# Performance work log

Measured on AMD Instinct MI355X. Metric: run time of the kernel, lower is better.

Reference implementation:

```python
import jax, jax.numpy as jnp
import numpy as np
import math

D_MODEL = 512
N_HEADS = 8
WINDOW = 5
B, S = 4, 2048


def setup_inputs() -> dict:
    key = jax.random.key(0)
    ks = jax.random.split(key, 16)
    d = D_MODEL

    def lin(k, fan_in, fan_out):
        bound = 1.0 / math.sqrt(fan_in)
        kw, kb = jax.random.split(k)
        W = jax.random.uniform(kw, (fan_in, fan_out), jnp.float32, -bound, bound)
        b = jax.random.uniform(kb, (fan_out,), jnp.float32, -bound, bound)
        return W, b

    x = jax.random.normal(ks[0], (B, S, d), jnp.float32)
    W1, b1 = lin(ks[1], d, 2 * d)      # mapping layer 1
    W2, b2 = lin(ks[2], 2 * d, d)      # mapping layer 2
    Wq, bq = lin(ks[3], d, d)
    Wk, bk = lin(ks[4], d, d)
    Wv, bv = lin(ks[5], d, d)
    Wo, bo = lin(ks[6], d, d)
    return dict(x=x, W1=W1, b1=b1, W2=W2, b2=b2, Wq=Wq, bq=bq,
                Wk=Wk, bk=bk, Wv=Wv, bv=bv, Wo=Wo, bo=bo)


def reference(x, W1, b1, W2, b2, Wq, bq, Wk, bk, Wv, bv, Wo, bo):
    Bsz, S_, d = x.shape
    h = N_HEADS
    hd = d // h

    # mapping MLP: Linear -> ReLU -> Linear
    xm = jax.nn.relu(x @ W1 + b1) @ W2 + b2

    def split_heads(t):  # [B,S,d] -> [B,h,S,hd]
        return t.reshape(Bsz, S_, h, hd).transpose(0, 2, 1, 3)

    Q = split_heads(xm @ Wq + bq)
    K = split_heads(xm @ Wk + bk)
    V = split_heads(xm @ Wv + bv)

    scores = jnp.einsum('bhqd,bhkd->bhqk', Q, K) / math.sqrt(hd)

    # inverse sliding-window mask: positions with |i-j| <= window are EXCLUDED
    idx = jnp.arange(S_)
    adjacent = jnp.abs(idx[:, None] - idx[None, :]) <= WINDOW  # [S,S] bool
    scores = jnp.where(adjacent[None, None], -1e9, scores)

    attn = jax.nn.softmax(scores, axis=-1)
    out = jnp.einsum('bhqk,bhkd->bhqd', attn, V)
    out = out.transpose(0, 2, 1, 3).reshape(Bsz, S_, d)
    return out @ Wo + bo
```

## Files before the change

kernel.cpp:

```cpp
#include <hip/hip_runtime.h>
#include <stdint.h>

typedef __attribute__((ext_vector_type(8))) short bf16x8;
typedef __attribute__((ext_vector_type(4))) float f32x4;

__device__ __forceinline__ float bf2f(uint16_t u) {
    union { uint32_t u; float f; } c; c.u = ((uint32_t)u) << 16; return c.f;
}
__device__ __forceinline__ uint16_t f2bf(float f) {
    union { float f; uint32_t u; } c; c.f = f;
    uint32_t r = c.u + 0x7fffu + ((c.u >> 16) & 1u);
    return (uint16_t)(r >> 16);
}
__device__ __forceinline__ uint32_t pk2bf(float a, float b) {
#if __has_builtin(__builtin_amdgcn_cvt_pk_bf16_f32)
    auto v = __builtin_amdgcn_cvt_pk_bf16_f32(a, b);
    uint32_t u; __builtin_memcpy(&u, &v, 4); return u;
#else
    return (uint32_t)f2bf(a) | ((uint32_t)f2bf(b) << 16);
#endif
}

__device__ __forceinline__ void gld_lds16(const uint16_t* g, uint16_t* l) {
    __builtin_amdgcn_global_load_lds(
        (const __attribute__((address_space(1))) void*)g,
        (__attribute__((address_space(3))) void*)l, 16, 0, 0);
}

__global__ void prep_all(const float* __restrict__ x,
                         const float* __restrict__ W1, const float* __restrict__ W2,
                         const float* __restrict__ Wq, const float* __restrict__ Wk,
                         const float* __restrict__ Wv, const float* __restrict__ Wo,
                         const float* __restrict__ b1, const float* __restrict__ b2,
                         const float* __restrict__ bq, const float* __restrict__ bk,
                         const float* __restrict__ bv, const float* __restrict__ bo,
                         uint16_t* __restrict__ W1T, uint16_t* __restrict__ W2T,
                         uint16_t* __restrict__ WqkvT, uint16_t* __restrict__ WoT,
                         uint16_t* __restrict__ xb, uint16_t* __restrict__ bbase)
{
    const int id = blockIdx.x;
    const int tx = threadIdx.x, ty = threadIdx.y;
    const int tid = ty * 32 + tx;
    if (id < 2048) {
        __shared__ uint16_t t[32][33];
        const float* src; uint16_t* dst; int R, C, tile;
        if      (id < 512)  { src = W1; dst = W1T;              R = 512;  C = 1024; tile = id; }
        else if (id < 1024) { src = W2; dst = W2T;              R = 1024; C = 512;  tile = id - 512; }
        else if (id < 1280) { src = Wq; dst = WqkvT;            R = 512;  C = 512;  tile = id - 1024; }
        else if (id < 1536) { src = Wk; dst = WqkvT + 512*512;  R = 512;  C = 512;  tile = id - 1280; }
        else if (id < 1792) { src = Wv; dst = WqkvT + 1024*512; R = 512;  C = 512;  tile = id - 1536; }
        else                { src = Wo; dst = WoT;              R = 512;  C = 512;  tile = id - 1792; }
        const int ntx = C / 32;
        const int bx = (tile % ntx) * 32, by = (tile / ntx) * 32;
#pragma unroll
        for (int i = ty; i < 32; i += 8) t[i][tx] = f2bf(src[(size_t)(by + i) * C + bx + tx]);
        __syncthreads();
#pragma unroll
        for (int i = ty; i < 32; i += 8) dst[(size_t)(bx + i) * R + by + tx] = t[tx][i];
    } else if (id < 6144) {
        int i = (id - 2048) * 256 + tid;
        float4 v = ((const float4*)x)[i];
        ushort4 o;
        o.x = f2bf(v.x); o.y = f2bf(v.y); o.z = f2bf(v.z); o.w = f2bf(v.w);
        ((ushort4*)xb)[i] = o;
    } else {
        int i = (id - 6144) * 256 + tid;
        if      (i < 1024) bbase[i] = f2bf(b1[i]);
        else if (i < 1536) bbase[i] = f2bf(b2[i - 1024]);
        else if (i < 2048) bbase[i] = f2bf(bq[i - 1536]);
        else if (i < 2560) bbase[i] = f2bf(bk[i - 2048]);
        else if (i < 3072) bbase[i] = f2bf(bv[i - 2560]);
        else if (i < 3584) bbase[i] = f2bf(bo[i - 3072]);
    }
}

template<int RELU, int F32OUT>
__global__ __launch_bounds__(256)
void gemm_k(const uint16_t* __restrict__ A, const uint16_t* __restrict__ Bt,
            const uint16_t* __restrict__ bias, void* __restrict__ Cv,
            int M, int N, int K)
{
    __shared__ __align__(16) uint16_t lsA[128 * 32];
    __shared__ __align__(16) uint16_t lsB[128 * 32];

    const int tid = threadIdx.x, lane = tid & 63, wid = tid >> 6;
    const int quad = lane >> 4, lm = lane & 15;
    const int wm = wid >> 1, wn = wid & 1;
    const int m0 = blockIdx.y * 128, n0 = blockIdx.x * 128;

    f32x4 acc[4][4];
#pragma unroll
    for (int i = 0; i < 4; ++i)
#pragma unroll
        for (int j = 0; j < 4; ++j) acc[i][j] = (f32x4){0.f, 0.f, 0.f, 0.f};

    const int row0 = tid >> 2, row1 = (256 + tid) >> 2, cg = tid & 3;

    for (int k0 = 0; k0 < K; k0 += 32) {
        __syncthreads();
        gld_lds16(A  + (size_t)(m0 + row0) * K + k0 + cg * 8, lsA + (size_t)tid * 8);
        gld_lds16(A  + (size_t)(m0 + row1) * K + k0 + cg * 8, lsA + (size_t)(256 + tid) * 8);
        gld_lds16(Bt + (size_t)(n0 + row0) * K + k0 + cg * 8, lsB + (size_t)tid * 8);
        gld_lds16(Bt + (size_t)(n0 + row1) * K + k0 + cg * 8, lsB + (size_t)(256 + tid) * 8);
        __syncthreads();

        bf16x8 af[4], bfr[4];
#pragma unroll
        for (int t = 0; t < 4; ++t) {
            af[t]  = *(const bf16x8*)(lsA + (wm * 64 + t * 16 + lm) * 32 + quad * 8);
            bfr[t] = *(const bf16x8*)(lsB + (wn * 64 + t * 16 + lm) * 32 + quad * 8);
        }
#pragma unroll
        for (int i = 0; i < 4; ++i)
#pragma unroll
            for (int j = 0; j < 4; ++j)
                acc[i][j] = __builtin_amdgcn_mfma_f32_16x16x32_bf16(af[i], bfr[j], acc[i][j], 0, 0, 0);
    }

#pragma unroll
    for (int i = 0; i < 4; ++i) {
        const int r0 = m0 + wm * 64 + i * 16 + quad * 4;
#pragma unroll
        for (int j = 0; j < 4; ++j) {
            const int col = n0 + wn * 64 + j * 16 + lm;
            const float bvj = bf2f(bias[col]);
#pragma unroll
            for (int r = 0; r < 4; ++r) {
                float v = acc[i][j][r] + bvj;
                if (RELU) v = fmaxf(v, 0.f);
                if (F32OUT) ((float*)Cv)[(size_t)(r0 + r) * N + col] = v;
                else        ((uint16_t*)Cv)[(size_t)(r0 + r) * N + col] = f2bf(v);
            }
        }
    }
}

template<int RELU, int F32OUT>
__global__ __launch_bounds__(256)
void gemm_k64(const uint16_t* __restrict__ A, const uint16_t* __restrict__ Bt,
              const uint16_t* __restrict__ bias, void* __restrict__ Cv,
              int M, int N, int K)
{
    __shared__ __align__(16) uint16_t lsA[64 * 32];
    __shared__ __align__(16) uint16_t lsB[128 * 32];

    const int tid = threadIdx.x, lane = tid & 63, wid = tid >> 6;
    const int quad = lane >> 4, lm = lane & 15;
    const int wm = wid >> 1, wn = wid & 1;
    const int m0 = blockIdx.y * 64, n0 = blockIdx.x * 128;

    f32x4 acc[2][4];
#pragma unroll
    for (int i = 0; i < 2; ++i)
#pragma unroll
        for (int j = 0; j < 4; ++j) acc[i][j] = (f32x4){0.f, 0.f, 0.f, 0.f};

    const int rowA = tid >> 2;
    const int rowB0 = tid >> 2, rowB1 = (256 + tid) >> 2, cg = tid & 3;

    for (int k0 = 0; k0 < K; k0 += 32) {
        __syncthreads();
        gld_lds16(A  + (size_t)(m0 + rowA) * K + k0 + cg * 8, lsA + (size_t)tid * 8);
        gld_lds16(Bt + (size_t)(n0 + rowB0) * K + k0 + cg * 8, lsB + (size_t)tid * 8);
        gld_lds16(Bt + (size_t)(n0 + rowB1) * K + k0 + cg * 8, lsB + (size_t)(256 + tid) * 8);
        __syncthreads();

        bf16x8 af[2], bfr[4];
#pragma unroll
        for (int t = 0; t < 2; ++t)
            af[t] = *(const bf16x8*)(lsA + (wm * 32 + t * 16 + lm) * 32 + quad * 8);
#pragma unroll
        for (int t = 0; t < 4; ++t)
            bfr[t] = *(const bf16x8*)(lsB + (wn * 64 + t * 16 + lm) * 32 + quad * 8);
#pragma unroll
        for (int i = 0; i < 2; ++i)
#pragma unroll
            for (int j = 0; j < 4; ++j)
                acc[i][j] = __builtin_amdgcn_mfma_f32_16x16x32_bf16(af[i], bfr[j], acc[i][j], 0, 0, 0);
    }

#pragma unroll
    for (int i = 0; i < 2; ++i) {
        const int r0 = m0 + wm * 32 + i * 16 + quad * 4;
#pragma unroll
        for (int j = 0; j < 4; ++j) {
            const int col = n0 + wn * 64 + j * 16 + lm;
            const float bvj = bf2f(bias[col]);
#pragma unroll
            for (int r = 0; r < 4; ++r) {
                float v = acc[i][j][r] + bvj;
                if (RELU) v = fmaxf(v, 0.f);
                if (F32OUT) ((float*)Cv)[(size_t)(r0 + r) * N + col] = v;
                else        ((uint16_t*)Cv)[(size_t)(r0 + r) * N + col] = f2bf(v);
            }
        }
    }
}

__global__ __launch_bounds__(256)
void gemm_qkv_s(const uint16_t* __restrict__ A, const uint16_t* __restrict__ Bt,
                const uint16_t* __restrict__ bq, const uint16_t* __restrict__ bk,
                const uint16_t* __restrict__ bv_,
                uint16_t* __restrict__ qk, uint16_t* __restrict__ Vt)
{
    __shared__ __align__(16) uint16_t lsA[128 * 32];
    __shared__ __align__(16) uint16_t lsB[128 * 32];

    const int tid = threadIdx.x, lane = tid & 63, wid = tid >> 6;
    const int quad = lane >> 4, lm = lane & 15;
    const int wm = wid >> 1, wn = wid & 1;
    const int m0 = blockIdx.y * 128, n0 = blockIdx.x * 128;
    const int part = n0 >> 9;
    const uint16_t* B = (part == 0) ? bq : (part == 1) ? bk : bv_;
    const int K = 512;

    f32x4 acc[4][4];
#pragma unroll
    for (int i = 0; i < 4; ++i)
#pragma unroll
        for (int j = 0; j < 4; ++j) acc[i][j] = (f32x4){0.f, 0.f, 0.f, 0.f};

    const int row0 = tid >> 2, row1 = (256 + tid) >> 2, cg = tid & 3;

    for (int k0 = 0; k0 < K; k0 += 32) {
        __syncthreads();
        gld_lds16(A  + (size_t)(m0 + row0) * K + k0 + cg * 8, lsA + (size_t)tid * 8);
        gld_lds16(A  + (size_t)(m0 + row1) * K + k0 + cg * 8, lsA + (size_t)(256 + tid) * 8);
        gld_lds16(Bt + (size_t)(n0 + row0) * K + k0 + cg * 8, lsB + (size_t)tid * 8);
        gld_lds16(Bt + (size_t)(n0 + row1) * K + k0 + cg * 8, lsB + (size_t)(256 + tid) * 8);
        __syncthreads();

        bf16x8 af[4], bfr[4];
#pragma unroll
        for (int t = 0; t < 4; ++t) {
            af[t]  = *(const bf16x8*)(lsA + (wm * 64 + t * 16 + lm) * 32 + quad * 8);
            bfr[t] = *(const bf16x8*)(lsB + (wn * 64 + t * 16 + lm) * 32 + quad * 8);
        }
#pragma unroll
        for (int i = 0; i < 4; ++i)
#pragma unroll
            for (int j = 0; j < 4; ++j)
                acc[i][j] = __builtin_amdgcn_mfma_f32_16x16x32_bf16(af[i], bfr[j], acc[i][j], 0, 0, 0);
    }

#pragma unroll
    for (int i = 0; i < 4; ++i) {
        const int mb = m0 + wm * 64 + i * 16 + quad * 4;
#pragma unroll
        for (int j = 0; j < 4; ++j) {
            const int nl = (n0 & 511) + wn * 64 + j * 16 + lm;
            const float bvj = bf2f(B[nl]);
            if (part < 2) {
#pragma unroll
                for (int r = 0; r < 4; ++r)
                    qk[(size_t)(mb + r) * 1024 + part * 512 + nl] = f2bf(acc[i][j][r] + bvj);
            } else {
                const int h = nl >> 6, d = nl & 63;
                const int b = mb >> 11, s0 = mb & 2047;
                const size_t base = ((size_t)(((b << 3) | h)) * 64 + d) * 2048 + s0;
#pragma unroll
                for (int r = 0; r < 4; ++r)
                    Vt[base + r] = f2bf(acc[i][j][r] + bvj);
            }
        }
    }
}

__global__ __launch_bounds__(256, 2)
void attn_k(const uint16_t* __restrict__ qk, const uint16_t* __restrict__ Vt,
            uint16_t* __restrict__ Out)
{
    __shared__ __align__(16) uint16_t lsK[128 * 64];
    __shared__ __align__(16) uint16_t lsV[64 * 128];
    __shared__ __align__(16) uint16_t lsP[128 * 136];

    const int tid = threadIdx.x, lane = tid & 63, wid = tid >> 6;
    const int quad = lane >> 4, lm = lane & 15;
    const int bh = blockIdx.y, b = bh >> 3, h = bh & 7;
    const int q0 = blockIdx.x * 128;
    const float cscale = 0.125f * 1.44269504088896f;

    bf16x8 qf[2][2];
#pragma unroll
    for (int i = 0; i < 2; ++i)
#pragma unroll
        for (int ks = 0; ks < 2; ++ks) {
            bf16x8 q = *(const bf16x8*)(qk +
                (size_t)(b * 2048 + q0 + wid * 32 + i * 16 + lm) * 1024 + h * 64 + ks * 32 + quad * 8);
#pragma unroll
            for (int e = 0; e < 8; ++e)
                q[e] = (short)f2bf(bf2f((uint16_t)q[e]) * cscale);
            qf[i][ks] = q;
        }

    f32x4 oacc[2][4];
#pragma unroll
    for (int i = 0; i < 2; ++i)
#pragma unroll
        for (int n = 0; n < 4; ++n) oacc[i][n] = (f32x4){0.f, 0.f, 0.f, 0.f};
    float lrow[2][4];
#pragma unroll
    for (int i = 0; i < 2; ++i)
#pragma unroll
        for (int r = 0; r < 4; ++r) lrow[i][r] = 0.f;

    for (int j0 = 0; j0 < 2048; j0 += 128) {
        __syncthreads();
#pragma unroll
        for (int c4 = 0; c4 < 4; ++c4) {
            const int chunk = c4 * 256 + tid;
            const int r = chunk >> 3, lc = (chunk & 7) ^ (r & 7);
            gld_lds16(qk + (size_t)(b * 2048 + j0 + r) * 1024 + 512 + h * 64 + lc * 8,
                      lsK + (size_t)chunk * 8);
        }
#pragma unroll
        for (int c4 = 0; c4 < 4; ++c4) {
            const int chunk = c4 * 256 + tid;
            const int d = chunk >> 4, lc = (chunk & 15) ^ (d & 15);
            gld_lds16(Vt + (size_t)(bh * 64 + d) * 2048 + j0 + lc * 8,
                      lsV + (size_t)chunk * 8);
        }
        __syncthreads();

        f32x4 sacc[2][8];
#pragma unroll
        for (int i = 0; i < 2; ++i)
#pragma unroll
            for (int j = 0; j < 8; ++j) sacc[i][j] = (f32x4){0.f, 0.f, 0.f, 0.f};
#pragma unroll
        for (int ks = 0; ks < 2; ++ks)
#pragma unroll
            for (int j = 0; j < 8; ++j) {
                const int pc = (ks * 4 + quad) ^ (lm & 7);
                bf16x8 kf = *(const bf16x8*)(lsK + (j * 16 + lm) * 64 + pc * 8);
#pragma unroll
                for (int i = 0; i < 2; ++i)
                    sacc[i][j] = __builtin_amdgcn_mfma_f32_16x16x32_bf16(qf[i][ks], kf, sacc[i][j], 0, 0, 0);
            }

        if ((j0 + 127 >= q0 - 5) && (j0 <= q0 + 127 + 5)) {
#pragma unroll
            for (int i = 0; i < 2; ++i)
#pragma unroll
                for (int j = 0; j < 8; ++j)
#pragma unroll
                    for (int r = 0; r < 4; ++r) {
                        int qr = q0 + wid * 32 + i * 16 + quad * 4 + r;
                        int kc = j0 + j * 16 + lm;
                        int dd = qr - kc; if (dd < 0) dd = -dd;
                        if (dd <= 5) sacc[i][j][r] = -1e30f;
                    }
        }

#pragma unroll
        for (int i = 0; i < 2; ++i)
#pragma unroll
            for (int r = 0; r < 4; ++r) {
                const int prow = wid * 32 + i * 16 + quad * 4 + r;
                float p[8], rs = 0.f;
#pragma unroll
                for (int j = 0; j < 8; ++j) { p[j] = exp2f(sacc[i][j][r]); rs += p[j]; }
                lrow[i][r] += rs;
#pragma unroll
                for (int jp = 0; jp < 4; ++jp) {
                    uint32_t u = pk2bf(p[2 * jp], p[2 * jp + 1]);
                    lsP[prow * 136 + (2 * jp) * 16 + lm]     = (uint16_t)u;
                    lsP[prow * 136 + (2 * jp + 1) * 16 + lm] = (uint16_t)(u >> 16);
                }
            }

#pragma unroll
        for (int ks = 0; ks < 4; ++ks) {
            bf16x8 pa[2];
#pragma unroll
            for (int i = 0; i < 2; ++i)
                pa[i] = *(const bf16x8*)(lsP + (wid * 32 + i * 16 + lm) * 136 + ks * 32 + quad * 8);
#pragma unroll
            for (int n = 0; n < 4; ++n) {
                const int pc = (ks * 4 + quad) ^ lm;
                bf16x8 vf = *(const bf16x8*)(lsV + (n * 16 + lm) * 128 + pc * 8);
#pragma unroll
                for (int i = 0; i < 2; ++i)
                    oacc[i][n] = __builtin_amdgcn_mfma_f32_16x16x32_bf16(pa[i], vf, oacc[i][n], 0, 0, 0);
            }
        }
    }

#pragma unroll
    for (int i = 0; i < 2; ++i)
#pragma unroll
        for (int r = 0; r < 4; ++r) {
            float l = lrow[i][r];
            l += __shfl_xor(l, 1, 16);
            l += __shfl_xor(l, 2, 16);
            l += __shfl_xor(l, 4, 16);
            l += __shfl_xor(l, 8, 16);
            const float inv = 1.f / (l + 1e-30f);
            const int s = q0 + wid * 32 + i * 16 + quad * 4 + r;
#pragma unroll
            for (int n = 0; n < 4; ++n)
                Out[(size_t)(b * 2048 + s) * 512 + h * 64 + n * 16 + lm] = f2bf(oacc[i][n][r] * inv);
        }
}

extern "C" void kernel_launch(void* const* d_in, const int* in_sizes, int n_in,
                              void* d_out, int out_size, void* d_ws, size_t ws_size,
                              hipStream_t stream)
{
    const float* x  = (const float*)d_in[0];
    const float* W1 = (const float*)d_in[1];
    const float* b1 = (const float*)d_in[2];
    const float* W2 = (const float*)d_in[3];
    const float* b2 = (const float*)d_in[4];
    const float* Wq = (const float*)d_in[5];
    const float* bq = (const float*)d_in[6];
    const float* Wk = (const float*)d_in[7];
    const float* bk = (const float*)d_in[8];
    const float* Wv = (const float*)d_in[9];
    const float* bv = (const float*)d_in[10];
    const float* Wo = (const float*)d_in[11];
    const float* bo = (const float*)d_in[12];
    (void)in_sizes; (void)n_in; (void)out_size; (void)ws_size;

    char* ws = (char*)d_ws;
    const size_t MiB = 1024 * 1024;
    uint16_t* xb    = (uint16_t*)(ws + 0);
    uint16_t* W1T   = (uint16_t*)(ws + 8 * MiB);
    uint16_t* W2T   = (uint16_t*)(ws + 9 * MiB);
    uint16_t* WqkvT = (uint16_t*)(ws + 10 * MiB);
    uint16_t* WoT   = (uint16_t*)(ws + 11 * MiB + 512 * 1024);
    uint16_t* bbase = (uint16_t*)(ws + 12 * MiB);
    uint16_t* b1b = bbase, *b2b = bbase + 1024, *bqb = bbase + 1536;
    uint16_t* bkb = bbase + 2048, *bvb = bbase + 2560, *bob = bbase + 3072;
    uint16_t* xm1   = (uint16_t*)(ws + 13 * MiB);
    uint16_t* xm    = (uint16_t*)(ws + 29 * MiB);
    uint16_t* qk    = xm1;
    uint16_t* att   = xm;
    uint16_t* Vt    = xb;

    prep_all<<<6158, dim3(32, 8), 0, stream>>>(x, W1, W2, Wq, Wk, Wv, Wo,
                                               b1, b2, bq, bk, bv, bo,
                                               W1T, W2T, WqkvT, WoT, xb, bbase);

    gemm_k<1,0>  <<<dim3(8, 64),  256, 0, stream>>>(xb,  W1T, b1b, xm1, 8192, 1024, 512);
    gemm_k64<0,0><<<dim3(4, 128), 256, 0, stream>>>(xm1, W2T, b2b, xm,  8192, 512, 1024);
    gemm_qkv_s   <<<dim3(12, 64), 256, 0, stream>>>(xm, WqkvT, bqb, bkb, bvb, qk, Vt);
    attn_k       <<<dim3(16, 32), 256, 0, stream>>>(qk, Vt, att);
    gemm_k64<0,1><<<dim3(4, 128), 256, 0, stream>>>(att, WoT, bob, d_out, 8192, 512, 512);
}
```

Before: 251.3 us.

## Double GEMM K-step to 64 with XOR-swizzled LDS, use native exp2

All three GEMM kernels now stage 64-wide K slices per iteration instead of 32, halving the number of barrier pairs per tile. The LDS layout is XOR-swizzled by row to avoid bank conflicts on the wider rows. The attention softmax switches to the raw hardware exp2 builtin, which skips the library's range handling. The cost is double the LDS footprint per block, which may reduce occupancy.

```diff
diff --git a/kernel.cpp b/kernel.cpp
--- a/kernel.cpp
+++ b/kernel.cpp
@@ -18,6 +18,13 @@
     uint32_t u; __builtin_memcpy(&u, &v, 4); return u;
 #else
     return (uint32_t)f2bf(a) | ((uint32_t)f2bf(b) << 16);
+#endif
+}
+__device__ __forceinline__ float fexp2(float x) {
+#if __has_builtin(__builtin_amdgcn_exp2f)
+    return __builtin_amdgcn_exp2f(x);
+#else
+    return exp2f(x);
 #endif
 }
 
@@ -80,10 +87,11 @@
             const uint16_t* __restrict__ bias, void* __restrict__ Cv,
             int M, int N, int K)
 {
-    __shared__ __align__(16) uint16_t lsA[128 * 32];
-    __shared__ __align__(16) uint16_t lsB[128 * 32];
-
-    const int tid = threadIdx.x, lane = tid & 63, wid = tid >> 6;
+    __shared__ __align__(16) uint16_t lsA[128 * 64];
+    __shared__ __align__(16) uint16_t lsB[128 * 64];
+
+    const int tid = threadIdx.x, lane = tid & 63;
+    const int wid = tid >> 6;
     const int quad = lane >> 4, lm = lane & 15;
     const int wm = wid >> 1, wn = wid & 1;
     const int m0 = blockIdx.y * 128, n0 = blockIdx.x * 128;
@@ -94,27 +102,32 @@
 #pragma unroll
         for (int j = 0; j < 4; ++j) acc[i][j] = (f32x4){0.f, 0.f, 0.f, 0.f};
 
-    const int row0 = tid >> 2, row1 = (256 + tid) >> 2, cg = tid & 3;
-
-    for (int k0 = 0; k0 < K; k0 += 32) {
-        __syncthreads();
-        gld_lds16(A  + (size_t)(m0 + row0) * K + k0 + cg * 8, lsA + (size_t)tid * 8);
-        gld_lds16(A  + (size_t)(m0 + row1) * K + k0 + cg * 8, lsA + (size_t)(256 + tid) * 8);
-        gld_lds16(Bt + (size_t)(n0 + row0) * K + k0 + cg * 8, lsB + (size_t)tid * 8);
-        gld_lds16(Bt + (size_t)(n0 + row1) * K + k0 + cg * 8, lsB + (size_t)(256 + tid) * 8);
-        __syncthreads();
-
-        bf16x8 af[4], bfr[4];
-#pragma unroll
-        for (int t = 0; t < 4; ++t) {
-            af[t]  = *(const bf16x8*)(lsA + (wm * 64 + t * 16 + lm) * 32 + quad * 8);
-            bfr[t] = *(const bf16x8*)(lsB + (wn * 64 + t * 16 + lm) * 32 + quad * 8);
-        }
-#pragma unroll
-        for (int i = 0; i < 4; ++i)
-#pragma unroll
-            for (int j = 0; j < 4; ++j)
-                acc[i][j] = __builtin_amdgcn_mfma_f32_16x16x32_bf16(af[i], bfr[j], acc[i][j], 0, 0, 0);
+    for (int k0 = 0; k0 < K; k0 += 64) {
+        __syncthreads();
+#pragma unroll
+        for (int c4 = 0; c4 < 4; ++c4) {
+            const int chunk = c4 * 256 + tid;
+            const int r = chunk >> 3, lc = (chunk & 7) ^ (r & 7);
+            gld_lds16(A  + (size_t)(m0 + r) * K + k0 + lc * 8, lsA + (size_t)chunk * 8);
+            gld_lds16(Bt + (size_t)(n0 + r) * K + k0 + lc * 8, lsB + (size_t)chunk * 8);
+        }
+        __syncthreads();
+
+#pragma unroll
+        for (int kh = 0; kh < 2; ++kh) {
+            bf16x8 af[4], bfr[4];
+#pragma unroll
+            for (int t = 0; t < 4; ++t) {
+                const int pcA = ((kh * 4 + quad) ^ (lm & 7));
+                af[t]  = *(const bf16x8*)(lsA + (wm * 64 + t * 16 + lm) * 64 + pcA * 8);
+                bfr[t] = *(const bf16x8*)(lsB + (wn * 64 + t * 16 + lm) * 64 + pcA * 8);
+            }
+#pragma unroll
+            for (int i = 0; i < 4; ++i)
+#pragma unroll
+                for (int j = 0; j < 4; ++j)
+                    acc[i][j] = __builtin_amdgcn_mfma_f32_16x16x32_bf16(af[i], bfr[j], acc[i][j], 0, 0, 0);
+        }
     }
 
 #pragma unroll
@@ -141,10 +154,11 @@
               const uint16_t* __restrict__ bias, void* __restrict__ Cv,
               int M, int N, int K)
 {
-    __shared__ __align__(16) uint16_t lsA[64 * 32];
-    __shared__ __align__(16) uint16_t lsB[128 * 32];
-
-    const int tid = threadIdx.x, lane = tid & 63, wid = tid >> 6;
+    __shared__ __align__(16) uint16_t lsA[64 * 64];
+    __shared__ __align__(16) uint16_t lsB[128 * 64];
+
+    const int tid = threadIdx.x, lane = tid & 63;
+    const int wid = tid >> 6;
     const int quad = lane >> 4, lm = lane & 15;
     const int wm = wid >> 1, wn = wid & 1;
     const int m0 = blockIdx.y * 64, n0 = blockIdx.x * 128;
@@ -155,28 +169,38 @@
 #pragma unroll
         for (int j = 0; j < 4; ++j) acc[i][j] = (f32x4){0.f, 0.f, 0.f, 0.f};
 
-    const int rowA = tid >> 2;
-    const int rowB0 = tid >> 2, rowB1 = (256 + tid) >> 2, cg = tid & 3;
-
-    for (int k0 = 0; k0 < K; k0 += 32) {
-        __syncthreads();
-        gld_lds16(A  + (size_t)(m0 + rowA) * K + k0 + cg * 8, lsA + (size_t)tid * 8);
-        gld_lds16(Bt + (size_t)(n0 + rowB0) * K + k0 + cg * 8, lsB + (size_t)tid * 8);
-        gld_lds16(Bt + (size_t)(n0 + rowB1) * K + k0 + cg * 8, lsB + (size_t)(256 + tid) * 8);
-        __syncthreads();
-
-        bf16x8 af[2], bfr[4];
-#pragma unroll
-        for (int t = 0; t < 2; ++t)
-            af[t] = *(const bf16x8*)(lsA + (wm * 32 + t * 16 + lm) * 32 + quad * 8);
-#pragma unroll
-        for (int t = 0; t < 4; ++t)
-            bfr[t] = *(const bf16x8*)(lsB + (wn * 64 + t * 16 + lm) * 32 + quad * 8);
-#pragma unroll
-        for (int i = 0; i < 2; ++i)
-#pragma unroll
-            for (int j = 0; j < 4; ++j)
-                acc[i][j] = __builtin_amdgcn_mfma_f32_16x16x32_bf16(af[i], bfr[j], acc[i][j], 0, 0, 0);
+    for (int k0 = 0; k0 < K; k0 += 64) {
+        __syncthreads();
+#pragma unroll
+        for (int c4 = 0; c4 < 2; ++c4) {
+            const int chunk = c4 * 256 + tid;
+            const int r = chunk >> 3, lc = (chunk & 7) ^ (r & 7);
+            gld_lds16(A + (size_t)(m0 + r) * K + k0 + lc * 8, lsA + (size_t)chunk * 8);
+        }
+#pragma unroll
+        for (int c4 = 0; c4 < 4; ++c4) {
+            const int chunk = c4 * 256 + tid;
+            const int r = chunk >> 3, lc = (chunk & 7) ^ (r & 7);
+            gld_lds16(Bt + (size_t)(n0 + r) * K + k0 + lc * 8, lsB + (size_t)chunk * 8);
+        }
+        __syncthreads();
+
+#pragma unroll
+        for (int kh = 0; kh < 2; ++kh) {
+            const int pc = ((kh * 4 + quad) ^ (lm & 7));
+            bf16x8 af[2], bfr[4];
+#pragma unroll
+            for (int t = 0; t < 2; ++t)
+                af[t] = *(const bf16x8*)(lsA + (wm * 32 + t * 16 + lm) * 64 + pc * 8);
+#pragma unroll
+            for (int t = 0; t < 4; ++t)
+                bfr[t] = *(const bf16x8*)(lsB + (wn * 64 + t * 16 + lm) * 64 + pc * 8);
+#pragma unroll
+            for (int i = 0; i < 2; ++i)
+#pragma unroll
+                for (int j = 0; j < 4; ++j)
+                    acc[i][j] = __builtin_amdgcn_mfma_f32_16x16x32_bf16(af[i], bfr[j], acc[i][j], 0, 0, 0);
+        }
     }
 
 #pragma unroll
@@ -203,10 +227,11 @@
                 const uint16_t* __restrict__ bv_,
                 uint16_t* __restrict__ qk, uint16_t* __restrict__ Vt)
 {
-    __shared__ __align__(16) uint16_t lsA[128 * 32];
-    __shared__ __align__(16) uint16_t lsB[128 * 32];
-
-    const int tid = threadIdx.x, lane = tid & 63, wid = tid >> 6;
+    __shared__ __align__(16) uint16_t lsA[128 * 64];
+    __shared__ __align__(16) uint16_t lsB[128 * 64];
+
+    const int tid = threadIdx.x, lane = tid & 63;
+    const int wid = tid >> 6;
     const int quad = lane >> 4, lm = lane & 15;
     const int wm = wid >> 1, wn = wid & 1;
     const int m0 = blockIdx.y * 128, n0 = blockIdx.x * 128;
@@ -220,27 +245,32 @@
 #pragma unroll
         for (int j = 0; j < 4; ++j) acc[i][j] = (f32x4){0.f, 0.f, 0.f, 0.f};
 
-    const int row0 = tid >> 2, row1 = (256 + tid) >> 2, cg = tid & 3;
-
-    for (int k0 = 0; k0 < K; k0 += 32) {
-        __syncthreads();
-        gld_lds16(A  + (size_t)(m0 + row0) * K + k0 + cg * 8, lsA + (size_t)tid * 8);
-        gld_lds16(A  + (size_t)(m0 + row1) * K + k0 + cg * 8, lsA + (size_t)(256 + tid) * 8);
-        gld_lds16(Bt + (size_t)(n0 + row0) * K + k0 + cg * 8, lsB + (size_t)tid * 8);
-        gld_lds16(Bt + (size_t)(n0 + row1) * K + k0 + cg * 8, lsB + (size_t)(256 + tid) * 8);
-        __syncthreads();
-
-        bf16x8 af[4], bfr[4];
-#pragma unroll
-        for (int t = 0; t < 4; ++t) {
-            af[t]  = *(const bf16x8*)(lsA + (wm * 64 + t * 16 + lm) * 32 + quad * 8);
-            bfr[t] = *(const bf16x8*)(lsB + (wn * 64 + t * 16 + lm) * 32 + quad * 8);
-        }
-#pragma unroll
-        for (int i = 0; i < 4; ++i)
-#pragma unroll
-            for (int j = 0; j < 4; ++j)
-                acc[i][j] = __builtin_amdgcn_mfma_f32_16x16x32_bf16(af[i], bfr[j], acc[i][j], 0, 0, 0);
+    for (int k0 = 0; k0 < K; k0 += 64) {
+        __syncthreads();
+#pragma unroll
+        for (int c4 = 0; c4 < 4; ++c4) {
+            const int chunk = c4 * 256 + tid;
+            const int r = chunk >> 3, lc = (chunk & 7) ^ (r & 7);
+            gld_lds16(A  + (size_t)(m0 + r) * K + k0 + lc * 8, lsA + (size_t)chunk * 8);
+            gld_lds16(Bt + (size_t)(n0 + r) * K + k0 + lc * 8, lsB + (size_t)chunk * 8);
+        }
+        __syncthreads();
+
+#pragma unroll
+        for (int kh = 0; kh < 2; ++kh) {
+            const int pc = ((kh * 4 + quad) ^ (lm & 7));
+            bf16x8 af[4], bfr[4];
+#pragma unroll
+            for (int t = 0; t < 4; ++t) {
+                af[t]  = *(const bf16x8*)(lsA + (wm * 64 + t * 16 + lm) * 64 + pc * 8);
+                bfr[t] = *(const bf16x8*)(lsB + (wn * 64 + t * 16 + lm) * 64 + pc * 8);
+            }
+#pragma unroll
+            for (int i = 0; i < 4; ++i)
+#pragma unroll
+                for (int j = 0; j < 4; ++j)
+                    acc[i][j] = __builtin_amdgcn_mfma_f32_16x16x32_bf16(af[i], bfr[j], acc[i][j], 0, 0, 0);
+        }
     }
 
 #pragma unroll
@@ -359,7 +389,7 @@
                 const int prow = wid * 32 + i * 16 + quad * 4 + r;
                 float p[8], rs = 0.f;
 #pragma unroll
-                for (int j = 0; j < 8; ++j) { p[j] = exp2f(sacc[i][j][r]); rs += p[j]; }
+                for (int j = 0; j < 8; ++j) { p[j] = fexp2(sacc[i][j][r]); rs += p[j]; }
                 lrow[i][r] += rs;
 #pragma unroll
                 for (int jp = 0; jp < 4; ++jp) {
```

Result: faster. 225.4 us (-10.3%).
